# Optimization experiments

Measured on AMD Instinct MI355X. Metric: run time of the kernel, lower is better.

## Reference

```python
import jax, jax.numpy as jnp
import numpy as np

NHEADS = 8
NEG_INF = -1e9


def setup_inputs() -> dict:
    key = jax.random.key(0)
    k1, k2, k3, k4 = jax.random.split(key, 4)
    B, Nq, Nk, E = 1024, 1, 512, 256
    return {
        "query": jax.random.normal(k1, (B, Nq, E), dtype=jnp.float32),
        "key": jax.random.normal(k2, (B, Nk, E), dtype=jnp.float32),
        "value": jax.random.normal(k3, (B, Nk, E), dtype=jnp.float32),
        "mask": jax.random.randint(k4, (B, Nk), 0, 2, dtype=jnp.int32),
        "clip": 10,
    }


def reference(query, key, value, mask, clip):
    B, Nq, E = query.shape
    Nk = key.shape[1]
    h = NHEADS
    dh = E // h
    # Head split: E is chopped into h contiguous chunks of dh (matches the
    # torch view on the (B, E, N) transposed tensor).
    q = query.reshape(B, Nq, h, dh)
    k = key.reshape(B, Nk, h, dh)
    v = value.reshape(B, Nk, h, dh)
    # scores: [B, h, Nq, Nk]
    scores = jnp.einsum("bqhd,bkhd->bhqk", q, k) / jnp.sqrt(jnp.float32(dh))
    # mask is per-key: (B, Nk) -> broadcast over heads and query positions
    scores = jnp.where(mask[:, None, None, :] == 1, jnp.float32(NEG_INF), scores)
    # tanh logit clipping (applied AFTER masking, as in the original)
    scores = clip * jnp.tanh(scores)
    attn_prob = jax.nn.softmax(scores, axis=-1)  # [B, h, Nq, Nk]
    attn = jnp.einsum("bhqk,bkhd->bqhd", attn_prob, v).reshape(B, Nq, E)
    # mean over heads: (B, h, 1, Nk) -> (B, 1, Nk)  (Nq == 1 required)
    attn_prob_mean = attn_prob.mean(axis=1)
    return attn, attn_prob_mean
```

## Files before the change

kernel.cpp:

```cpp
#include <hip/hip_runtime.h>


constexpr int NB = 1024;
constexpr int NK = 512;
constexpr int E  = 256;
constexpr int H  = 8;
constexpr int PAD_NK = NK + 4;

__global__ __launch_bounds__(256, 4)
void mha_kernel(const float* __restrict__ q,
                const float* __restrict__ kmat,
                const float* __restrict__ vmat,
                const int* __restrict__ mask,
                const int* __restrict__ clip_p,
                float* __restrict__ out_attn,
                float* __restrict__ out_prob)
{
    __shared__ float  s_sc[H][PAD_NK];
    __shared__ float4 s_part[4][64];
    __shared__ float  s_sums[4][H];
    __shared__ int    s_mask[NK];
    __shared__ int    s_idx[4][128];

    const int b    = blockIdx.x;
    const int tid  = threadIdx.x;
    const int lane = tid & 63;
    const int wave = tid >> 6;
    const int h    = lane >> 3;

    const float clipf = (float)(*clip_p);
    const float scale = 0.17677669529663687f;
    const float pmask = __expf(-clipf);

    for (int i = tid; i < NK; i += 256) s_mask[i] = mask[(size_t)b * NK + i];
    const float4 qf = *reinterpret_cast<const float4*>(q + (size_t)b * E + lane * 4);
    const float* kb = kmat + (size_t)b * NK * E;
    const float* vb = vmat + (size_t)b * NK * E;
    __syncthreads();

    int cnt = 0;
    #pragma unroll
    for (int half = 0; half < 2; ++half) {
        const int k  = wave * 128 + half * 64 + lane;
        const bool un = (s_mask[k] != 1);
        const unsigned long long bal = __ballot(un);
        const int pos = __popcll(bal & ((1ull << lane) - 1ull));
        if (un) s_idx[wave][cnt + pos] = k;
        cnt += (int)__popcll(bal);
    }

    float4 acc = make_float4(0.f, 0.f, 0.f, 0.f);
    float  psum = 0.f;
    int j = 0;
    for (; j + 8 <= cnt; j += 8) {
        int idx[8];
        #pragma unroll
        for (int u = 0; u < 8; ++u) idx[u] = s_idx[wave][j + u];
        float4 kf[8];
        #pragma unroll
        for (int u = 0; u < 8; ++u)
            kf[u] = *reinterpret_cast<const float4*>(kb + (size_t)idx[u] * E + lane * 4);
        float p[8];
        #pragma unroll
        for (int u = 0; u < 8; ++u) {
            float s = kf[u].x * qf.x + kf[u].y * qf.y + kf[u].z * qf.z + kf[u].w * qf.w;
            s += __shfl_xor(s, 1);
            s += __shfl_xor(s, 2);
            s += __shfl_xor(s, 4);
            float sc = fminf(fmaxf(s * scale, -20.f), 20.f);
            const float ex = __expf(2.f * sc);
            const float th = (ex - 1.f) / (ex + 1.f);
            p[u] = __expf(clipf * th);
            if ((lane & 7) == 0) s_sc[h][idx[u]] = p[u];
            psum += p[u];
        }
        float4 vf[8];
        #pragma unroll
        for (int u = 0; u < 8; ++u)
            vf[u] = *reinterpret_cast<const float4*>(vb + (size_t)idx[u] * E + lane * 4);
        #pragma unroll
        for (int u = 0; u < 8; ++u) {
            acc.x += p[u] * vf[u].x; acc.y += p[u] * vf[u].y;
            acc.z += p[u] * vf[u].z; acc.w += p[u] * vf[u].w;
        }
    }
    for (; j < cnt; ++j) {
        const int kk = s_idx[wave][j];
        const float4 kf = *reinterpret_cast<const float4*>(kb + (size_t)kk * E + lane * 4);
        float s = kf.x * qf.x + kf.y * qf.y + kf.z * qf.z + kf.w * qf.w;
        s += __shfl_xor(s, 1);
        s += __shfl_xor(s, 2);
        s += __shfl_xor(s, 4);
        float sc = fminf(fmaxf(s * scale, -20.f), 20.f);
        const float ex = __expf(2.f * sc);
        const float th = (ex - 1.f) / (ex + 1.f);
        const float p = __expf(clipf * th);
        if ((lane & 7) == 0) s_sc[h][kk] = p;
        psum += p;
        const float4 vf = *reinterpret_cast<const float4*>(vb + (size_t)kk * E + lane * 4);
        acc.x += p * vf.x; acc.y += p * vf.y; acc.z += p * vf.z; acc.w += p * vf.w;
    }
    psum += (float)(128 - cnt) * pmask;

    if ((lane & 7) == 0) s_sums[wave][h] = psum;
    s_part[wave][lane] = acc;
    __syncthreads();

    float inv[H];
    #pragma unroll
    for (int hh = 0; hh < H; ++hh)
        inv[hh] = 1.0f / (s_sums[0][hh] + s_sums[1][hh] + s_sums[2][hh] + s_sums[3][hh]);
    float invsum = 0.f;
    #pragma unroll
    for (int hh = 0; hh < H; ++hh) invsum += inv[hh];

    for (int k = tid; k < NK; k += 256) {
        float o;
        if (s_mask[k] == 1) {
            o = pmask * invsum * 0.125f;
        } else {
            float s = 0.f;
            #pragma unroll
            for (int hh = 0; hh < H; ++hh) s += s_sc[hh][k] * inv[hh];
            o = s * 0.125f;
        }
        out_prob[(size_t)b * NK + k] = o;
    }

    if (tid < 64) {
        const float4 r0 = s_part[0][tid], r1 = s_part[1][tid],
                     r2 = s_part[2][tid], r3 = s_part[3][tid];
        const float iv = inv[tid >> 3];
        float4 o;
        o.x = (r0.x + r1.x + r2.x + r3.x) * iv;
        o.y = (r0.y + r1.y + r2.y + r3.y) * iv;
        o.z = (r0.z + r1.z + r2.z + r3.z) * iv;
        o.w = (r0.w + r1.w + r2.w + r3.w) * iv;
        *reinterpret_cast<float4*>(out_attn + (size_t)b * E + tid * 4) = o;
    }
}

extern "C" void kernel_launch(void* const* d_in, const int* in_sizes, int n_in,
                              void* d_out, int out_size, void* d_ws, size_t ws_size,
                              hipStream_t stream) {
    const float* q    = (const float*)d_in[0];
    const float* kmat = (const float*)d_in[1];
    const float* vmat = (const float*)d_in[2];
    const int*   mask = (const int*)d_in[3];
    const int*   clip = (const int*)d_in[4];

    float* out_attn = (float*)d_out;
    float* out_prob = (float*)d_out + (size_t)NB * E;

    mha_kernel<<<dim3(NB), dim3(256), 0, stream>>>(q, kmat, vmat, mask, clip,
                                                   out_attn, out_prob);
}
```

Measured before the change: 108.4 us.

## Balance unmasked keys across waves and split K and V passes

```diff
diff --git a/kernel.cpp b/kernel.cpp
--- a/kernel.cpp
+++ b/kernel.cpp
@@ -19,8 +19,8 @@
     __shared__ float  s_sc[H][PAD_NK];
     __shared__ float4 s_part[4][64];
     __shared__ float  s_sums[4][H];
-    __shared__ int    s_mask[NK];
-    __shared__ int    s_idx[4][128];
+    __shared__ int    s_idx[NK];
+    __shared__ int    s_cnt[8];
 
     const int b    = blockIdx.x;
     const int tid  = threadIdx.x;
@@ -32,35 +32,52 @@
     const float scale = 0.17677669529663687f;
     const float pmask = __expf(-clipf);
 
-    for (int i = tid; i < NK; i += 256) s_mask[i] = mask[(size_t)b * NK + i];
     const float4 qf = *reinterpret_cast<const float4*>(q + (size_t)b * E + lane * 4);
     const float* kb = kmat + (size_t)b * NK * E;
     const float* vb = vmat + (size_t)b * NK * E;
+
+    const int k0c = wave * 128 + lane;
+    const int k1c = wave * 128 + 64 + lane;
+    const bool un0 = (mask[(size_t)b * NK + k0c] != 1);
+    const bool un1 = (mask[(size_t)b * NK + k1c] != 1);
+    const unsigned long long bal0 = __ballot(un0);
+    const unsigned long long bal1 = __ballot(un1);
+    if (lane == 0) {
+        s_cnt[2 * wave]     = (int)__popcll(bal0);
+        s_cnt[2 * wave + 1] = (int)__popcll(bal1);
+    }
+    for (int i = tid; i < H * PAD_NK; i += 256)
+        ((float*)s_sc)[i] = pmask;
     __syncthreads();
 
-    int cnt = 0;
-    #pragma unroll
-    for (int half = 0; half < 2; ++half) {
-        const int k  = wave * 128 + half * 64 + lane;
-        const bool un = (s_mask[k] != 1);
-        const unsigned long long bal = __ballot(un);
-        const int pos = __popcll(bal & ((1ull << lane) - 1ull));
-        if (un) s_idx[wave][cnt + pos] = k;
-        cnt += (int)__popcll(bal);
+    int base[8];
+    {
+        int run = 0;
+        #pragma unroll
+        for (int c = 0; c < 8; ++c) { base[c] = run; run += s_cnt[c]; }
     }
+    const int total = base[7] + s_cnt[7];
+    {
+        const int pos0 = (int)__popcll(bal0 & ((1ull << lane) - 1ull));
+        if (un0) s_idx[base[2 * wave] + pos0] = k0c;
+        const int pos1 = (int)__popcll(bal1 & ((1ull << lane) - 1ull));
+        if (un1) s_idx[base[2 * wave + 1] + pos1] = k1c;
+    }
+    __syncthreads();
 
-    float4 acc = make_float4(0.f, 0.f, 0.f, 0.f);
-    float  psum = 0.f;
-    int j = 0;
-    for (; j + 8 <= cnt; j += 8) {
+    const int lo = (total * wave) >> 2;
+    const int hi = (total * (wave + 1)) >> 2;
+
+    float psum = 0.f;
+    int j = lo;
+    for (; j + 8 <= hi; j += 8) {
         int idx[8];
         #pragma unroll
-        for (int u = 0; u < 8; ++u) idx[u] = s_idx[wave][j + u];
+        for (int u = 0; u < 8; ++u) idx[u] = s_idx[j + u];
         float4 kf[8];
         #pragma unroll
         for (int u = 0; u < 8; ++u)
             kf[u] = *reinterpret_cast<const float4*>(kb + (size_t)idx[u] * E + lane * 4);
-        float p[8];
         #pragma unroll
         for (int u = 0; u < 8; ++u) {
             float s = kf[u].x * qf.x + kf[u].y * qf.y + kf[u].z * qf.z + kf[u].w * qf.w;
@@ -70,22 +87,13 @@
             float sc = fminf(fmaxf(s * scale, -20.f), 20.f);
             const float ex = __expf(2.f * sc);
             const float th = (ex - 1.f) / (ex + 1.f);
-            p[u] = __expf(clipf * th);
-            if ((lane & 7) == 0) s_sc[h][idx[u]] = p[u];
-            psum += p[u];
-        }
-        float4 vf[8];
-        #pragma unroll
-        for (int u = 0; u < 8; ++u)
-            vf[u] = *reinterpret_cast<const float4*>(vb + (size_t)idx[u] * E + lane * 4);
-        #pragma unroll
-        for (int u = 0; u < 8; ++u) {
-            acc.x += p[u] * vf[u].x; acc.y += p[u] * vf[u].y;
-            acc.z += p[u] * vf[u].z; acc.w += p[u] * vf[u].w;
+            const float p  = __expf(clipf * th);
+            if ((lane & 7) == 0) s_sc[h][idx[u]] = p;
+            psum += p;
         }
     }
-    for (; j < cnt; ++j) {
-        const int kk = s_idx[wave][j];
+    for (; j < hi; ++j) {
+        const int kk = s_idx[j];
         const float4 kf = *reinterpret_cast<const float4*>(kb + (size_t)kk * E + lane * 4);
         float s = kf.x * qf.x + kf.y * qf.y + kf.z * qf.z + kf.w * qf.w;
         s += __shfl_xor(s, 1);
@@ -97,35 +105,49 @@
         const float p = __expf(clipf * th);
         if ((lane & 7) == 0) s_sc[h][kk] = p;
         psum += p;
-        const float4 vf = *reinterpret_cast<const float4*>(vb + (size_t)kk * E + lane * 4);
-        acc.x += p * vf.x; acc.y += p * vf.y; acc.z += p * vf.z; acc.w += p * vf.w;
     }
-    psum += (float)(128 - cnt) * pmask;
-
     if ((lane & 7) == 0) s_sums[wave][h] = psum;
-    s_part[wave][lane] = acc;
     __syncthreads();
 
+    const float mterm = (float)(NK - total) * pmask;
     float inv[H];
     #pragma unroll
     for (int hh = 0; hh < H; ++hh)
-        inv[hh] = 1.0f / (s_sums[0][hh] + s_sums[1][hh] + s_sums[2][hh] + s_sums[3][hh]);
-    float invsum = 0.f;
-    #pragma unroll
-    for (int hh = 0; hh < H; ++hh) invsum += inv[hh];
+        inv[hh] = 1.0f / (s_sums[0][hh] + s_sums[1][hh] + s_sums[2][hh] +
+                          s_sums[3][hh] + mterm);
+
+    float4 acc = make_float4(0.f, 0.f, 0.f, 0.f);
+    j = lo;
+    for (; j + 8 <= hi; j += 8) {
+        int idx[8];
+        #pragma unroll
+        for (int u = 0; u < 8; ++u) idx[u] = s_idx[j + u];
+        float4 vf[8];
+        #pragma unroll
+        for (int u = 0; u < 8; ++u)
+            vf[u] = *reinterpret_cast<const float4*>(vb + (size_t)idx[u] * E + lane * 4);
+        #pragma unroll
+        for (int u = 0; u < 8; ++u) {
+            const float p = s_sc[h][idx[u]];
+            acc.x += p * vf[u].x; acc.y += p * vf[u].y;
+            acc.z += p * vf[u].z; acc.w += p * vf[u].w;
+        }
+    }
+    for (; j < hi; ++j) {
+        const int kk = s_idx[j];
+        const float4 vf = *reinterpret_cast<const float4*>(vb + (size_t)kk * E + lane * 4);
+        const float p = s_sc[h][kk];
+        acc.x += p * vf.x; acc.y += p * vf.y; acc.z += p * vf.z; acc.w += p * vf.w;
+    }
+    s_part[wave][lane] = acc;
 
     for (int k = tid; k < NK; k += 256) {
-        float o;
-        if (s_mask[k] == 1) {
-            o = pmask * invsum * 0.125f;
-        } else {
-            float s = 0.f;
-            #pragma unroll
-            for (int hh = 0; hh < H; ++hh) s += s_sc[hh][k] * inv[hh];
-            o = s * 0.125f;
-        }
-        out_prob[(size_t)b * NK + k] = o;
+        float s = 0.f;
+        #pragma unroll
+        for (int hh = 0; hh < H; ++hh) s += s_sc[hh][k] * inv[hh];
+        out_prob[(size_t)b * NK + k] = s * 0.125f;
     }
+    __syncthreads();
 
     if (tid < 64) {
         const float4 r0 = s_part[0][tid], r1 = s_part[1][tid],
```

New measurement: 104.9 us (median of 2 runs). 3.2% less time.
